# Kernel tuning notes

Hardware: AMD Instinct MI355X
Metric: run time of the kernel (lower is better)

Reference implementation:

```python
import jax, jax.numpy as jnp
import numpy as np

B, N, R, S, FIN, NCLS, KNN = 16, 2048, 64, 64, 6, 40, 40


def _knn_laplacian(x, k):
    # pairwise squared distance -> gaussian affinity -> row-wise top-k sparsify
    # -> symmetric-normalized Laplacian  L = I - D^{-1/2} A D^{-1/2}
    xx = jnp.sum(x * x, axis=-1)                      # [B,N]
    inner = jnp.einsum('bnd,bmd->bnm', x, x)          # [B,N,N]
    dist = xx[:, :, None] + xx[:, None, :] - 2.0 * inner
    A = jnp.exp(-dist)
    kth = jax.lax.top_k(A, k)[0][..., -1]             # k-th largest per row [B,N]
    A = jnp.where(A >= kth[..., None], A, jnp.zeros((), A.dtype))
    d = jnp.sum(A, axis=-1)
    dis = jnp.where(d > 0, jax.lax.rsqrt(jnp.maximum(d, 1e-12)), jnp.zeros((), A.dtype))
    L = jnp.eye(A.shape[-1], dtype=A.dtype) - dis[:, :, None] * A * dis[:, None, :]
    return L


def _cheb_conv(x, L, w, b):
    # DenseChebConv, K=3: T0=x, T1=Lx, T2=2LT1-T0, then linear on concat
    t0 = x
    t1 = jnp.matmul(L, x)
    t2 = 2.0 * jnp.matmul(L, t1) - t0
    xc = jnp.concatenate([t0, t1, t2], axis=-1)       # [B,N,3*Fin]
    return jnp.matmul(xc, w) + b


def setup_inputs() -> dict:
    key = jax.random.key(0)
    ks = jax.random.split(key, 16)
    p = lambda k_, sh: (jax.random.normal(k_, sh, dtype=jnp.float32) * 0.02)
    return {
        'x': jax.random.normal(ks[0], (B, N, FIN), dtype=jnp.float32),
        'laplacian_Reeb': jax.random.normal(ks[1], (B, R, R), dtype=jnp.float32),
        'sccs': jax.random.randint(ks[2], (B, R, S), 0, N),
        'vertices_reeb': jax.random.normal(ks[3], (B * R, 3), dtype=jnp.float32),
        'edges_reeb': jax.random.randint(ks[4], (B, 128, 2), 0, R),
        'labels': jax.random.randint(ks[5], (B,), 0, NCLS),
        'k': KNN, 'batch_size': B, 'num_points': N,
        'conv1_w': p(ks[6], (3 * FIN, 128)), 'conv1_b': jnp.zeros((128,), jnp.float32),
        'conv2_w': p(ks[7], (3 * 128, 512)), 'conv2_b': jnp.zeros((512,), jnp.float32),
        'convReeb_w': p(ks[8], (3 * 128, 512)), 'convReeb_b': jnp.zeros((512,), jnp.float32),
        'fc1_w': p(ks[9], (1024, 512)), 'fc1_b': jnp.zeros((512,), jnp.float32),
        'fc2_w': p(ks[10], (512, 128)), 'fc2_b': jnp.zeros((128,), jnp.float32),
        'fc3_w': p(ks[11], (128, NCLS)), 'fc3_b': jnp.zeros((NCLS,), jnp.float32),
    }


def reference(x, laplacian_Reeb, sccs, vertices_reeb, edges_reeb, labels, k,
              batch_size, num_points, conv1_w, conv1_b, conv2_w, conv2_b,
              convReeb_w, convReeb_b, fc1_w, fc1_b, fc2_w, fc2_b, fc3_w, fc3_b):
    regs = []
    # graph build is under no_grad in the original
    L = jax.lax.stop_gradient(_knn_laplacian(x, k))
    out = jax.nn.relu(_cheb_conv(x, L, conv1_w, conv1_b))           # [B,N,128]
    regs.append(jnp.linalg.norm(jnp.einsum('bnf,bnm,bmg->bfg', out, L, out)) ** 2)

    # Reeb ragged segment-max pool (no_grad in original): gather SCC index
    # groups per Reeb node and max-reduce -> [B,R,128]
    gathered = jax.vmap(lambda o, s: o[s])(out, sccs)               # [B,R,S,128]
    Vertices_final_Reeb = jax.lax.stop_gradient(jnp.max(gathered, axis=2))
    laplacian_Reeb_final = jax.lax.stop_gradient(laplacian_Reeb)

    L2 = jax.lax.stop_gradient(_knn_laplacian(out, k))
    out = jax.nn.relu(_cheb_conv(out, L2, conv2_w, conv2_b))        # [B,N,512]
    regs.append(jnp.linalg.norm(jnp.einsum('bnf,bnm,bmg->bfg', out, L2, out)) ** 2)

    out_Reeb = jax.nn.relu(_cheb_conv(Vertices_final_Reeb, laplacian_Reeb_final,
                                      convReeb_w, convReeb_b))      # [B,R,512]
    regs.append(jnp.linalg.norm(jnp.einsum('brf,brq,bqg->bfg', out_Reeb,
                                           laplacian_Reeb_final, out_Reeb)) ** 2)

    out = jnp.max(out, axis=1)            # [B,512]
    out_Reeb = jnp.max(out_Reeb, axis=1)  # [B,512]
    out = jnp.concatenate([out_Reeb, out], axis=1)                  # [B,1024]

    out = jnp.matmul(out, fc1_w) + fc1_b
    regs.append(jnp.linalg.norm(fc1_w[:, 0]) ** 2); regs.append(fc1_b[0] ** 2)
    out = jax.nn.relu(out)
    out = jnp.matmul(out, fc2_w) + fc2_b
    regs.append(jnp.linalg.norm(fc2_w[:, 0]) ** 2); regs.append(fc2_b[0] ** 2)
    out = jax.nn.relu(out)
    out = jnp.matmul(out, fc3_w) + fc3_b
    regs.append(jnp.linalg.norm(fc3_w[:, 0]) ** 2); regs.append(fc3_b[0] ** 2)
    return out, jnp.stack(regs)
```

## Files before the change

### kernel.cpp

```cpp
#include <hip/hip_runtime.h>

#define NB 16
#define NP 2048
#define NR 64
#define NS 64
#define KSEL 40

typedef __attribute__((ext_vector_type(8))) short bf16x8;
typedef __attribute__((ext_vector_type(4))) float f32x4;

constexpr long aOUT1 = 0;
constexpr long aT1A  = aOUT1 + 16L*2048*128;
constexpr long aT2A  = aT1A  + 16L*2048*6;
constexpr long aZ1   = aT2A  + 16L*2048*6;
constexpr long aVALS1= aZ1   + 16L*2048*128;
constexpr long aDIS1 = aVALS1+ 16L*2048*64;
constexpr long aVALS2= aDIS1 + 16L*2048;
constexpr long aDIS2 = aVALS2+ 16L*2048*64;
constexpr long aXX2  = aDIS2 + 16L*2048;
constexpr long aXX1  = aXX2  + 16L*2048;
constexpr long aT1B  = aXX1  + 16L*2048;
constexpr long aT2B  = aT1B  + 16L*2048*128;
constexpr long aOUT2 = aT2B  + 16L*2048*128;
constexpr long aZ2   = aOUT2 + 16L*2048*512;
constexpr long aVFR  = aZ2   + 16L*2048*512;
constexpr long aT1R  = aVFR  + 16L*64*128;
constexpr long aT2R  = aT1R  + 16L*64*128;
constexpr long aOUTR = aT2R  + 16L*64*128;
constexpr long aZR   = aOUTR + 16L*64*512;
constexpr long aPOOL = aZR   + 16L*64*512;
constexpr long aFC1O = aPOOL + 16L*1024;
constexpr long aFC2O = aFC1O + 16L*512;
constexpr long aMPP  = aFC2O + 16L*128;
constexpr long aM1P  = aMPP  + 16L*8*512;
constexpr long aM2P  = aM1P  + 8L*16*128*128;
constexpr long FTOT  = aM2P  + 4L*16*512*512;

constexpr long iCOLS1 = 0;
constexpr long iCNT1  = iCOLS1 + 16L*2048*64;
constexpr long iCOLS2 = iCNT1  + 16L*2048;
constexpr long iCNT2  = iCOLS2 + 16L*2048*64;
constexpr long ITOT   = iCNT2  + 16L*2048;

constexpr long uOUT1H = 0;
constexpr long uOUT1L = uOUT1H + 16L*2048*128;
constexpr long uOUT1R = uOUT1L + 16L*2048*128;
constexpr long uT1BH  = uOUT1R + 16L*2048*128;
constexpr long uT1BL  = uT1BH  + 16L*2048*128;
constexpr long uT2BH  = uT1BL  + 16L*2048*128;
constexpr long uT2BL  = uT2BH  + 16L*2048*128;
constexpr long uW2T   = uT2BL  + 16L*2048*128;
constexpr long uVFRH  = uW2T   + 512L*384;
constexpr long uVFRL  = uVFRH  + 16L*64*128;
constexpr long uT1RH  = uVFRL  + 16L*64*128;
constexpr long uT1RL  = uT1RH  + 16L*64*128;
constexpr long uT2RH  = uT1RL  + 16L*64*128;
constexpr long uT2RL  = uT2RH  + 16L*64*128;
constexpr long uWRT   = uT2RL  + 16L*64*128;
constexpr long uOUT1T = uWRT   + 512L*384;
constexpr long uZ1T   = uOUT1T + 16L*128*2048;
constexpr long uOUT2T = uZ1T   + 16L*128*2048;
constexpr long uZ2T   = uOUT2T + 16L*512*2048;
constexpr long uOUTRT = uZ2T   + 16L*512*2048;
constexpr long uZRT   = uOUTRT + 16L*512*64;
constexpr long uOUT2B = uZRT   + 16L*512*64;
constexpr long uG     = uOUT2B + 16L*2048*512;
constexpr long UTOT   = uG     + 16L*2048*2048;

__device__ __align__(256) float  g_farena[FTOT];
__device__ __align__(256) int    g_iarena[ITOT];
__device__ __align__(256) ushort g_uarena[UTOT];

__device__ __forceinline__ float wsum_f(float v){
  #pragma unroll
  for (int s=32;s>0;s>>=1) v += __shfl_xor(v, s, 64);
  return v;
}
__device__ __forceinline__ int wsum_i(int v){
  #pragma unroll
  for (int s=32;s>0;s>>=1) v += __shfl_xor(v, s, 64);
  return v;
}

__device__ __forceinline__ void gl2lds16(const void* g, void* l){
  __builtin_amdgcn_global_load_lds(
      (const __attribute__((address_space(1))) void*)g,
      (__attribute__((address_space(3))) void*)l, 16, 0, 0);
}

__device__ __forceinline__ ushort bf_rne(float x){
  unsigned u = __float_as_uint(x);
  u += 0x7fffu + ((u >> 16) & 1u);
  return (ushort)(u >> 16);
}
__device__ __forceinline__ void bf_hilo(float x, ushort& h, ushort& l){
  unsigned u = __float_as_uint(x);
  h = (ushort)(u >> 16);
  float hf = __uint_as_float(u & 0xffff0000u);
  l = (ushort)(__float_as_uint(x - hf) >> 16);
}
__device__ __forceinline__ float bf2f(ushort u){
  return __uint_as_float(((unsigned)u) << 16);
}

__device__ __forceinline__ void topk_store(float (&dk)[32], int lane, long row,
    int* __restrict__ cols, float* __restrict__ vals,
    int* __restrict__ cnt, float* __restrict__ dis)
{
  float dmin = dk[0], dmax = dk[0];
  #pragma unroll
  for (int q=1;q<32;++q){ dmin = fminf(dmin, dk[q]); dmax = fmaxf(dmax, dk[q]); }
  #pragma unroll
  for (int s=32;s>0;s>>=1){
    dmin = fminf(dmin, __shfl_xor(dmin, s, 64));
    dmax = fmaxf(dmax, __shfl_xor(dmax, s, 64));
  }
  int c0 = 0;
  #pragma unroll
  for (int q=0;q<32;++q) c0 += (int)__popcll(__ballot(dk[q] <= dmin));
  float kth;
  if (c0 >= KSEL){
    kth = dmin;
  } else {
    float lo = dmin, hi = dmax;
    int cLo = c0, cHi = 2048, it = 0;
    while (cHi != KSEL && __float_as_uint(hi) - __float_as_uint(lo) > 1u){
      float t;
      if (it & 1){
        t = __uint_as_float((__float_as_uint(lo) + __float_as_uint(hi)) >> 1);
      } else {
        t = lo + (hi - lo) * ((float)(KSEL - cLo) / (float)(cHi - cLo));
        unsigned tb = __float_as_uint(t);
        unsigned lb = __float_as_uint(lo), hb = __float_as_uint(hi);
        if (tb <= lb) tb = lb + 1u;
        else if (tb >= hb) tb = hb - 1u;
        t = __uint_as_float(tb);
      }
      ++it;
      int c = 0;
      #pragma unroll
      for (int q=0;q<32;++q) c += (int)__popcll(__ballot(dk[q] <= t));
      if (c >= KSEL){ hi = t; cHi = c; } else { lo = t; cLo = c; }
    }
    kth = hi;
  }
  int kc = 0;
  #pragma unroll
  for (int q=0;q<32;++q) kc += (dk[q] <= kth) ? 1 : 0;
  int tot = wsum_i(kc);
  int incl = kc;
  #pragma unroll
  for (int s=1;s<64;s<<=1){ int u = __shfl_up(incl, s, 64); if (lane >= s) incl += u; }
  int pos = incl - kc;
  int* cp = cols + row*64; float* vp = vals + row*64;
  float d = 0.f;
  #pragma unroll
  for (int q=0;q<32;++q){
    if (dk[q] <= kth){
      float v = __expf(-dk[q]);
      d += v;
      if (pos < 64){ cp[pos] = q*64 + lane; vp[pos] = v; }
      pos++;
    }
  }
  d = wsum_f(d);
  if (lane == 0){
    cnt[row] = tot <= 64 ? tot : 64;
    dis[row] = d > 0.f ? (1.0f / sqrtf(fmaxf(d, 1e-12f))) : 0.f;
  }
}

__global__ __launch_bounds__(256) void xx6_kernel(const float* __restrict__ x,
    float* __restrict__ xx1)
{
  long i = (long)blockIdx.x*256 + threadIdx.x;
  const float* p = x + i*6;
  float2 v0 = *(const float2*)(p);
  float2 v1 = *(const float2*)(p+2);
  float2 v2 = *(const float2*)(p+4);
  xx1[i] = v0.x*v0.x + v0.y*v0.y + v1.x*v1.x + v1.y*v1.y + v2.x*v2.x + v2.y*v2.y;
}

__global__ __launch_bounds__(256) void knn1_kernel(const float* __restrict__ x,
    const float* __restrict__ xx1,
    int* __restrict__ cols, float* __restrict__ vals, int* __restrict__ cnt,
    float* __restrict__ dis)
{
  int lane = threadIdx.x & 63;
  long row = (long)blockIdx.x*4 + (threadIdx.x >> 6);
  int b = (int)(row >> 11); int i = (int)(row & (NP-1));
  const float* xb = x + (long)b*NP*6;
  const float* xxb = xx1 + ((long)b << 11);
  float xi[6];
  #pragma unroll
  for (int d2=0; d2<6; ++d2) xi[d2] = xb[(long)i*6 + d2];
  float xxi = xxb[i];
  float dk[32];
  #pragma unroll 4
  for (int c=0;c<32;++c){
    int j = c*64 + lane;
    const float* xj = xb + (long)j*6;
    float2 v0 = *(const float2*)(xj);
    float2 v1 = *(const float2*)(xj+2);
    float2 v2 = *(const float2*)(xj+4);
    float inr = xi[0]*v0.x + xi[1]*v0.y + xi[2]*v1.x + xi[3]*v1.y + xi[4]*v2.x + xi[5]*v2.y;
    dk[c] = fmaxf(xxi + xxb[j] - 2.f*inr, 0.f);
  }
  topk_store(dk, lane, row, cols, vals, cnt, dis);
}

__global__ __launch_bounds__(256) void knn2_kernel(const ushort* __restrict__ G,
    const float* __restrict__ xx,
    int* __restrict__ cols, float* __restrict__ vals, int* __restrict__ cnt,
    float* __restrict__ dis)
{
  int lane = threadIdx.x & 63;
  long row = (long)blockIdx.x*4 + (threadIdx.x >> 6);
  const ushort* Gr = G + row*NP;
  const float* xxb = xx + ((row >> 11) << 11);
  int i = (int)(row & (NP-1));
  float xxi = xxb[i];
  float dk[32];
  #pragma unroll 4
  for (int c=0;c<32;++c){
    int j = c*64 + lane;
    dk[c] = fmaxf(xxi + xxb[j] - 2.f*bf2f(Gr[j]), 0.f);
  }
  topk_store(dk, lane, row, cols, vals, cnt, dis);
}

__global__ __launch_bounds__(256) void spmm6_kernel(const float* __restrict__ X,
    const float* __restrict__ T0, float* __restrict__ Y,
    const int* __restrict__ cols, const float* __restrict__ vals,
    const int* __restrict__ cnt, const float* __restrict__ dis,
    float c1, float c2, float cs)
{
  long row = (long)blockIdx.x*256 + threadIdx.x;
  int b = (int)(row >> 11);
  const float* Xb = X + ((long)b << 11)*6;
  const float* db = dis + ((long)b << 11);
  float acc[6] = {0,0,0,0,0,0};
  int c = cnt[row];
  const int* cp = cols + row*64; const float* vp = vals + row*64;
  for (int t=0;t<c;++t){
    int j = cp[t];
    float w = vp[t] * db[j];
    const float* xr = Xb + (long)j*6;
    #pragma unroll
    for (int d2=0; d2<6; ++d2) acc[d2] += w * xr[d2];
  }
  float di = dis[row];
  #pragma unroll
  for (int d2=0; d2<6; ++d2)
    Y[row*6+d2] = c1*X[row*6+d2] + c2*T0[row*6+d2] - cs*di*acc[d2];
}

template<int W, bool PACK>
__global__ __launch_bounds__((W >= 256) ? 256 : W) void spmm_kernel(
    const float* __restrict__ X, const float* __restrict__ T0, float* __restrict__ Y,
    ushort* __restrict__ Hh, ushort* __restrict__ Ll,
    const int* __restrict__ cols, const float* __restrict__ vals,
    const int* __restrict__ cnt, const float* __restrict__ dis,
    float c1, float c2, float cs)
{
  constexpr int TPB = (W >= 256) ? 256 : W;
  constexpr int E = W / TPB;
  __shared__ int scol[64];
  __shared__ float sval[64];
  int q = blockIdx.x;
  long row = ((long)(q & 7) << 12) + (q >> 3);
  int b = (int)(row >> 11);
  int tid = threadIdx.x;
  int c = cnt[row];
  if (tid < 64){ scol[tid] = cols[row*64+tid]; sval[tid] = vals[row*64+tid]; }
  __syncthreads();
  const float* Xb = X + ((long)b << 11)*W;
  const float* db = dis + ((long)b << 11);
  float acc[E] = {};
  for (int t=0;t<c;++t){
    int j = scol[t];
    float w = sval[t] * db[j];
    const float* xr = Xb + (long)j*W;
    #pragma unroll
    for (int e=0;e<E;++e) acc[e] += w * xr[tid + e*TPB];
  }
  float di = dis[row];
  #pragma unroll
  for (int e=0;e<E;++e){
    long idx = row*W + tid + e*TPB;
    float y = c1*X[idx] + c2*T0[idx] - cs*di*acc[e];
    Y[idx] = y;
    if (PACK){
      ushort h, l; bf_hilo(y, h, l);
      Hh[idx] = h; Ll[idx] = l;
    }
  }
}

__global__ __launch_bounds__(256) void spmmb_kernel(
    const float* __restrict__ X, const ushort* __restrict__ Xb,
    float* __restrict__ Y,
    const int* __restrict__ cols, const float* __restrict__ vals,
    const int* __restrict__ cnt, const float* __restrict__ dis)
{
  __shared__ int scol[4][64];
  __shared__ float sval[4][64];
  int q = blockIdx.x;
  int wid = threadIdx.x >> 6, lane = threadIdx.x & 63;
  long row = ((long)(q & 7) << 12) + ((long)(q >> 3) << 2) + wid;
  int b = (int)(row >> 11);
  scol[wid][lane] = cols[row*64 + lane];
  sval[wid][lane] = vals[row*64 + lane];
  const ushort* Xbb = Xb + ((long)b << 11)*512;
  const float* db = dis + ((long)b << 11);
  int c = cnt[row];
  float acc[8] = {};
  for (int t=0;t<c;++t){
    int j = scol[wid][t];
    float w = sval[wid][t] * db[j];
    bf16x8 v = *(const bf16x8*)(Xbb + (long)j*512 + lane*8);
    #pragma unroll
    for (int e=0;e<8;++e)
      acc[e] += w * bf2f((ushort)v[e]);
  }
  float di = dis[row];
  long base = row*512 + lane*8;
  float4 x0 = *(const float4*)(X + base);
  float4 x1 = *(const float4*)(X + base + 4);
  float4 o0, o1;
  o0.x = x0.x - di*acc[0]; o0.y = x0.y - di*acc[1];
  o0.z = x0.z - di*acc[2]; o0.w = x0.w - di*acc[3];
  o1.x = x1.x - di*acc[4]; o1.y = x1.y - di*acc[5];
  o1.z = x1.z - di*acc[6]; o1.w = x1.w - di*acc[7];
  *(float4*)(Y + base) = o0;
  *(float4*)(Y + base + 4) = o1;
}

__global__ __launch_bounds__(128) void conv1_kernel(const float* __restrict__ x,
    const float* __restrict__ t1, const float* __restrict__ t2,
    const float* __restrict__ w, const float* __restrict__ bias,
    float* __restrict__ out, ushort* __restrict__ oh, ushort* __restrict__ ol,
    ushort* __restrict__ orr)
{
  long row = blockIdx.x; int o = threadIdx.x;
  float acc = bias[o];
  const float* xr = x + row*6; const float* a1 = t1 + row*6; const float* a2 = t2 + row*6;
  #pragma unroll
  for (int d2=0; d2<6; ++d2){
    acc += xr[d2]*w[d2*128 + o];
    acc += a1[d2]*w[(6+d2)*128 + o];
    acc += a2[d2]*w[(12+d2)*128 + o];
  }
  acc = fmaxf(acc, 0.f);
  long idx = row*128 + o;
  out[idx] = acc;
  ushort h, l; bf_hilo(acc, h, l);
  oh[idx] = h; ol[idx] = l;
  orr[idx] = bf_rne(acc);
}

template<bool HILO>
__global__ __launch_bounds__(256) void tpack_kernel(const float* __restrict__ X,
    ushort* __restrict__ H, ushort* __restrict__ L,
    int R, int C, long sIn, long sOut)
{
  __shared__ float tile[32][33];
  int c0 = blockIdx.x*32, r0 = blockIdx.y*32, b = blockIdx.z;
  const float* Xb = X + (long)b*sIn;
  int tx = threadIdx.x & 31, ty = threadIdx.x >> 5;
  #pragma unroll
  for (int rr=ty; rr<32; rr+=8)
    tile[rr][tx] = Xb[(long)(r0+rr)*C + c0+tx];
  __syncthreads();
  #pragma unroll
  for (int cc=ty; cc<32; cc+=8){
    float xv = tile[tx][cc];
    long oidx = (long)b*sOut + (long)(c0+cc)*R + r0 + tx;
    if (HILO){
      ushort h, l; bf_hilo(xv, h, l);
      H[oidx] = h; L[oidx] = l;
    } else {
      H[oidx] = bf_rne(xv);
    }
  }
}

template<bool SPLITA, bool CHEB, bool BR>
__global__ __launch_bounds__(256) void mgemm_kernel(
    const ushort* __restrict__ Ah0, const ushort* __restrict__ Ah1, const ushort* __restrict__ Ah2,
    const ushort* __restrict__ Al0, const ushort* __restrict__ Al1, const ushort* __restrict__ Al2,
    const ushort* __restrict__ Bh,
    const float* __restrict__ bias, float* __restrict__ C,
    ushort* __restrict__ Cb, float* __restrict__ ssq,
    int M, int N, int K, long sA, long sB, long sC,
    int kchunk, long sSplit)
{
  __shared__ ushort AsH[128*32];
  __shared__ ushort BsH[128*32];
  __shared__ ushort AsL[SPLITA ? 128*32 : 8];
  int bz = blockIdx.z;
  int kb = 0, ke = K;
  long coff = 0;
  if (kchunk > 0){
    int split = bz >> 4; bz &= 15;
    kb = split * kchunk;
    ke = kb + kchunk; if (ke > K) ke = K;
    coff = (long)split * sSplit;
  }
  int m0 = blockIdx.x*128, n0 = blockIdx.y*128;
  int tid = threadIdx.x, lane = tid & 63, wid = tid >> 6;
  int wm = (wid & 1)*64, wn = (wid >> 1)*64;
  f32x4 acc[4][4] = {};
  const ushort* Bb = Bh + (long)bz*sB;
  const ushort* Ab = CHEB ? Ah0 : (Ah0 + (long)bz*sA);
  const ushort* Alb = (SPLITA && !CHEB) ? (Al0 + (long)bz*sA) : Al0;

  for (int k0 = kb; k0 < ke; k0 += 32){
    #pragma unroll
    for (int cc2=0; cc2<2; ++cc2){
      int chunk = wid*2 + cc2;
      int e = chunk*512 + lane*8;
      int row = e >> 5;
      int slot = (e >> 3) & 3;
      int scol = (slot ^ ((row >> 1) & 3)) * 8;
      const ushort* asrc;
      if (CHEB){
        int kg2 = k0 + scol;
        const ushort* base = (kg2 < 128) ? Ah0 : ((kg2 < 256) ? Ah1 : Ah2);
        asrc = base + (long)(m0+row)*128 + (kg2 & 127);
      } else {
        asrc = Ab + (long)(m0+row)*K + k0 + scol;
      }
      gl2lds16(asrc, &AsH[chunk*512]);
      gl2lds16(Bb + (long)(n0+row)*K + k0 + scol, &BsH[chunk*512]);
      if (SPLITA){
        const ushort* alsrc;
        if (CHEB){
          int kg2 = k0 + scol;
          const ushort* base = (kg2 < 128) ? Al0 : ((kg2 < 256) ? Al1 : Al2);
          alsrc = base + (long)(m0+row)*128 + (kg2 & 127);
        } else {
          alsrc = Alb + (long)(m0+row)*K + k0 + scol;
        }
        gl2lds16(alsrc, &AsL[chunk*512]);
      }
    }
    __syncthreads();
    int lr = lane & 15, kg = lane >> 4;
    bf16x8 af[4], bfr[4];
    #pragma unroll
    for (int f=0; f<4; ++f){
      int ra = wm + f*16 + lr;
      int rb = wn + f*16 + lr;
      af[f]  = *(const bf16x8*)&AsH[ra*32 + (kg ^ ((ra>>1)&3))*8];
      bfr[f] = *(const bf16x8*)&BsH[rb*32 + (kg ^ ((rb>>1)&3))*8];
    }
    if (SPLITA){
      bf16x8 al[4];
      #pragma unroll
      for (int f=0; f<4; ++f){
        int ra = wm + f*16 + lr;
        al[f] = *(const bf16x8*)&AsL[ra*32 + (kg ^ ((ra>>1)&3))*8];
      }
      #pragma unroll
      for (int mf=0; mf<4; ++mf)
        #pragma unroll
        for (int nf=0; nf<4; ++nf){
          acc[mf][nf] = __builtin_amdgcn_mfma_f32_16x16x32_bf16(af[mf], bfr[nf], acc[mf][nf], 0,0,0);
          acc[mf][nf] = __builtin_amdgcn_mfma_f32_16x16x32_bf16(al[mf], bfr[nf], acc[mf][nf], 0,0,0);
        }
    } else {
      #pragma unroll
      for (int mf=0; mf<4; ++mf)
        #pragma unroll
        for (int nf=0; nf<4; ++nf)
          acc[mf][nf] = __builtin_amdgcn_mfma_f32_16x16x32_bf16(af[mf], bfr[nf], acc[mf][nf], 0,0,0);
    }
    __syncthreads();
  }
  int lr = lane & 15, l4 = (lane >> 4)*4;
  if (ssq){
    float s = 0.f;
    #pragma unroll
    for (int mf=0; mf<4; ++mf)
      #pragma unroll
      for (int nf=0; nf<4; ++nf)
        #pragma unroll
        for (int r=0; r<4; ++r){ float v = acc[mf][nf][r]; s += v*v; }
    s = wsum_f(s);
    if (lane == 0) atomicAdd(ssq, s);
    return;
  }
  #pragma unroll
  for (int mf=0; mf<4; ++mf){
    #pragma unroll
    for (int nf=0; nf<4; ++nf){
      int n = n0 + wn + nf*16 + lr;
      float bv = BR ? bias[n] : 0.f;
      #pragma unroll
      for (int r=0; r<4; ++r){
        int m = m0 + wm + mf*16 + l4 + r;
        float v = acc[mf][nf][r];
        if (BR) v = fmaxf(v + bv, 0.f);
        if (C)  C[coff + (long)bz*sC + (long)m*N + n] = v;
        if (Cb) Cb[(long)bz*sC + (long)m*N + n] = bf_rne(v);
      }
    }
  }
}

__global__ __launch_bounds__(256) void redssq_kernel(const float* __restrict__ P,
    long n, int S, long stride, float* __restrict__ tgt)
{
  __shared__ float ps[4];
  float s = 0.f;
  for (long i = (long)blockIdx.x*256 + threadIdx.x; i < n; i += (long)gridDim.x*256){
    float v = 0.f;
    for (int q=0;q<S;++q) v += P[i + (long)q*stride];
    s += v*v;
  }
  s = wsum_f(s);
  int lane = threadIdx.x & 63, wid = threadIdx.x >> 6;
  if (lane == 0) ps[wid] = s;
  __syncthreads();
  if (threadIdx.x == 0) atomicAdd(tgt, ps[0]+ps[1]+ps[2]+ps[3]);
}

__global__ __launch_bounds__(256) void rownorm_kernel(const float* __restrict__ X,
    float* __restrict__ xx)
{
  int lane = threadIdx.x & 63;
  long row = (long)blockIdx.x*4 + (threadIdx.x >> 6);
  const float* p = X + row*128;
  float v0 = p[lane], v1 = p[64+lane];
  float s = wsum_f(v0*v0 + v1*v1);
  if (lane == 0) xx[row] = s;
}

__global__ __launch_bounds__(128) void reeb_pool_kernel(const float* __restrict__ out1,
    const int* __restrict__ sccs, float* __restrict__ VfR,
    ushort* __restrict__ Hh, ushort* __restrict__ Ll)
{
  int q = blockIdx.x;
  int br = ((q & 7) << 7) + (q >> 3);
  int b = br >> 6;
  int f = threadIdx.x;
  const int* sp = sccs + (long)br*NS;
  const float* ob = out1 + ((long)b << 11)*128;
  float m = -1e30f;
  for (int s=0;s<NS;++s){
    int idx = sp[s];
    m = fmaxf(m, ob[(long)idx*128 + f]);
  }
  long oidx = (long)br*128 + f;
  VfR[oidx] = m;
  ushort h, l; bf_hilo(m, h, l);
  Hh[oidx] = h; Ll[oidx] = l;
}

template<int W, bool PACK>
__global__ __launch_bounds__((W>=256)?256:W) void reeb_mm_kernel(const float* __restrict__ Lap,
    const float* __restrict__ X, const float* __restrict__ T0, float* __restrict__ Y,
    ushort* __restrict__ Hh, ushort* __restrict__ Ll,
    float cs, float c2)
{
  constexpr int TPB = (W>=256)?256:W;
  constexpr int E = W/TPB;
  int br = blockIdx.x; int b = br >> 6; int r = br & 63;
  const float* lr = Lap + ((long)b*NR + r)*NR;
  const float* Xb = X + (long)b*NR*W;
  int tid = threadIdx.x;
  float acc[E] = {};
  for (int q=0;q<NR;++q){
    float w = lr[q];
    #pragma unroll
    for (int e=0;e<E;++e) acc[e] += w * Xb[(long)q*W + tid + e*TPB];
  }
  #pragma unroll
  for (int e=0;e<E;++e){
    long idx = (long)br*W + tid + e*TPB;
    float y = cs*acc[e] + c2*T0[idx];
    Y[idx] = y;
    if (PACK){
      ushort h, l; bf_hilo(y, h, l);
      Hh[idx] = h; Ll[idx] = l;
    }
  }
}

__global__ __launch_bounds__(512) void maxpool1_kernel(const float* __restrict__ X,
    float* __restrict__ part)
{
  int b = blockIdx.x, rc = blockIdx.y; int f = threadIdx.x;
  const float* p = X + ((long)b*2048 + (long)rc*256)*512 + f;
  float m = -1e30f;
  #pragma unroll 4
  for (int r=0;r<256;++r) m = fmaxf(m, p[(long)r*512]);
  part[((long)b*8+rc)*512 + f] = m;
}

__global__ __launch_bounds__(512) void maxpool2_kernel(const float* __restrict__ part,
    const float* __restrict__ outR, float* __restrict__ pool)
{
  int b = blockIdx.x; int f = threadIdx.x;
  const float* pp = part + (long)b*8*512 + f;
  float m = -1e30f;
  #pragma unroll
  for (int r=0;r<8;++r) m = fmaxf(m, pp[r*512]);
  pool[(long)b*1024 + 512 + f] = m;
  const float* rp = outR + (long)b*64*512 + f;
  float mr = -1e30f;
  #pragma unroll 4
  for (int r=0;r<64;++r) mr = fmaxf(mr, rp[(long)r*512]);
  pool[(long)b*1024 + f] = mr;
}

template<bool RELU>
__global__ __launch_bounds__(256) void fc_kernel(const float* __restrict__ in,
    const float* __restrict__ W, const float* __restrict__ bias,
    float* __restrict__ out, int IN, int OUT)
{
  __shared__ float red[4][64];
  int b = blockIdx.x, o0 = blockIdx.y*64;
  int tid = threadIdx.x;
  int ol = tid & 63, q = tid >> 6;
  int o = o0 + ol;
  const float* ip = in + (long)b*IN;
  float acc = 0.f;
  if (o < OUT){
    int kb = IN >> 2;
    int ks = q*kb;
    for (int i=0;i<kb;i+=8){
      #pragma unroll
      for (int u=0;u<8;++u){
        int k = ks + i + u;
        acc += ip[k]*W[(long)k*OUT + o];
      }
    }
  }
  red[q][ol] = acc;
  __syncthreads();
  if (tid < 64){
    int oo = o0 + tid;
    if (oo < OUT){
      float s = red[0][tid]+red[1][tid]+red[2][tid]+red[3][tid] + bias[oo];
      out[(long)b*OUT + oo] = RELU ? fmaxf(s, 0.f) : s;
    }
  }
}

__global__ __launch_bounds__(256) void wreg_kernel(const float* __restrict__ w1,
    const float* __restrict__ b1, const float* __restrict__ w2, const float* __restrict__ b2,
    const float* __restrict__ w3, const float* __restrict__ b3, float* __restrict__ out9)
{
  __shared__ float ps[3][4];
  int tid = threadIdx.x, lane = tid & 63, wid = tid >> 6;
  float s1 = 0.f, s2 = 0.f, s3 = 0.f;
  for (int i=tid;i<1024;i+=256){ float v = w1[(long)i*512]; s1 += v*v; }
  for (int i=tid;i<512;i+=256){ float v = w2[(long)i*128]; s2 += v*v; }
  if (tid < 128){ float v = w3[(long)tid*40]; s3 = v*v; }
  s1 = wsum_f(s1); s2 = wsum_f(s2); s3 = wsum_f(s3);
  if (lane == 0){ ps[0][wid]=s1; ps[1][wid]=s2; ps[2][wid]=s3; }
  __syncthreads();
  if (tid == 0){
    out9[3] = ps[0][0]+ps[0][1]+ps[0][2]+ps[0][3];
    out9[4] = b1[0]*b1[0];
    out9[5] = ps[1][0]+ps[1][1]+ps[1][2]+ps[1][3];
    out9[6] = b2[0]*b2[0];
    out9[7] = ps[2][0]+ps[2][1]+ps[2][2]+ps[2][3];
    out9[8] = b3[0]*b3[0];
  }
}

extern "C" void kernel_launch(void* const* d_in, const int* in_sizes, int n_in,
                              void* d_out, int out_size, void* d_ws, size_t ws_size,
                              hipStream_t stream)
{
  (void)in_sizes; (void)n_in; (void)d_ws; (void)ws_size; (void)out_size;
  const float* x    = (const float*)d_in[0];
  const float* lapR = (const float*)d_in[1];
  const int*   sccs = (const int*)d_in[2];
  const float* w1   = (const float*)d_in[9];
  const float* b1   = (const float*)d_in[10];
  const float* w2   = (const float*)d_in[11];
  const float* b2   = (const float*)d_in[12];
  const float* wR   = (const float*)d_in[13];
  const float* bRb  = (const float*)d_in[14];
  const float* fw1  = (const float*)d_in[15];
  const float* fb1  = (const float*)d_in[16];
  const float* fw2  = (const float*)d_in[17];
  const float* fb2  = (const float*)d_in[18];
  const float* fw3  = (const float*)d_in[19];
  const float* fb3  = (const float*)d_in[20];
  float* out = (float*)d_out;

  float* Fb = nullptr; int* Ib = nullptr; ushort* Ub = nullptr;
  hipGetSymbolAddress((void**)&Fb, HIP_SYMBOL(g_farena));
  hipGetSymbolAddress((void**)&Ib, HIP_SYMBOL(g_iarena));
  hipGetSymbolAddress((void**)&Ub, HIP_SYMBOL(g_uarena));

  float* out1 = Fb + aOUT1;  float* t1a = Fb + aT1A;  float* t2a = Fb + aT2A;
  float* Z1   = Fb + aZ1;
  float* vals1= Fb + aVALS1; float* dis1= Fb + aDIS1;
  float* vals2= Fb + aVALS2; float* dis2= Fb + aDIS2;
  float* xx2  = Fb + aXX2;   float* xx1 = Fb + aXX1;
  float* t1b  = Fb + aT1B;   float* t2b = Fb + aT2B;
  float* out2 = Fb + aOUT2;  float* Z2  = Fb + aZ2;
  float* VfR  = Fb + aVFR;   float* t1R = Fb + aT1R;  float* t2R= Fb + aT2R;
  float* outR = Fb + aOUTR;  float* ZR  = Fb + aZR;
  float* pool = Fb + aPOOL;  float* fc1o= Fb + aFC1O; float* fc2o=Fb + aFC2O;
  float* mpp  = Fb + aMPP;   float* M1p = Fb + aM1P;  float* M2p = Fb + aM2P;
  int* cols1 = Ib + iCOLS1; int* cnt1 = Ib + iCNT1;
  int* cols2 = Ib + iCOLS2; int* cnt2 = Ib + iCNT2;
  ushort* out1h = Ub + uOUT1H; ushort* out1l = Ub + uOUT1L;
  ushort* out1r = Ub + uOUT1R;
  ushort* t1bh  = Ub + uT1BH;  ushort* t1bl  = Ub + uT1BL;
  ushort* t2bh  = Ub + uT2BH;  ushort* t2bl  = Ub + uT2BL;
  ushort* w2t   = Ub + uW2T;
  ushort* vfrh  = Ub + uVFRH;  ushort* vfrl  = Ub + uVFRL;
  ushort* t1rh  = Ub + uT1RH;  ushort* t1rl  = Ub + uT1RL;
  ushort* t2rh  = Ub + uT2RH;  ushort* t2rl  = Ub + uT2RL;
  ushort* wrt   = Ub + uWRT;
  ushort* out1t = Ub + uOUT1T; ushort* z1t   = Ub + uZ1T;
  ushort* out2t = Ub + uOUT2T; ushort* z2t   = Ub + uZ2T;
  ushort* outrt = Ub + uOUTRT; ushort* zrt   = Ub + uZRT;
  ushort* out2b = Ub + uOUT2B; ushort* Gb16  = Ub + uG;

  hipMemsetAsync(out + 640, 0, 9*sizeof(float), stream);

  xx6_kernel<<<dim3(128),dim3(256),0,stream>>>(x, xx1);
  knn1_kernel<<<dim3(8192),dim3(256),0,stream>>>(x, xx1, cols1, vals1, cnt1, dis1);
  spmm6_kernel<<<dim3(128),dim3(256),0,stream>>>(x, x, t1a, cols1, vals1, cnt1, dis1, 1.f, 0.f, 1.f);
  spmm6_kernel<<<dim3(128),dim3(256),0,stream>>>(t1a, x, t2a, cols1, vals1, cnt1, dis1, 2.f, -1.f, 2.f);
  conv1_kernel<<<dim3(32768),dim3(128),0,stream>>>(x, t1a, t2a, w1, b1, out1, out1h, out1l, out1r);

  spmm_kernel<128,false><<<dim3(32768),dim3(128),0,stream>>>(out1, out1, Z1, nullptr, nullptr,
      cols1, vals1, cnt1, dis1, 1.f, 0.f, 1.f);
  tpack_kernel<false><<<dim3(4,64,16),dim3(256),0,stream>>>(out1, out1t, nullptr, 2048,128, 2048L*128, 128L*2048);
  tpack_kernel<false><<<dim3(4,64,16),dim3(256),0,stream>>>(Z1,   z1t,   nullptr, 2048,128, 2048L*128, 128L*2048);
  mgemm_kernel<false,false,false><<<dim3(1,1,128),dim3(256),0,stream>>>(
      out1t,nullptr,nullptr, nullptr,nullptr,nullptr, z1t, nullptr, M1p,
      nullptr, nullptr, 128,128,2048, 128L*2048, 128L*2048, 128L*128, 256, 16L*128*128);
  redssq_kernel<<<dim3(512),dim3(256),0,stream>>>(M1p, 16L*128*128, 8, 16L*128*128, out+640);
  reeb_pool_kernel<<<dim3(1024),dim3(128),0,stream>>>(out1, sccs, VfR, vfrh, vfrl);

  rownorm_kernel<<<dim3(8192),dim3(256),0,stream>>>(out1, xx2);
  mgemm_kernel<false,false,false><<<dim3(16,16,16),dim3(256),0,stream>>>(
      out1r,nullptr,nullptr, nullptr,nullptr,nullptr, out1r, nullptr, nullptr,
      Gb16, nullptr, 2048,2048,128, (long)NP*128, (long)NP*128, (long)NP*NP, 0, 0);
  knn2_kernel<<<dim3(8192),dim3(256),0,stream>>>(Gb16, xx2, cols2, vals2, cnt2, dis2);

  spmm_kernel<128,true><<<dim3(32768),dim3(128),0,stream>>>(out1, out1, t1b, t1bh, t1bl,
      cols2, vals2, cnt2, dis2, 1.f, 0.f, 1.f);
  spmm_kernel<128,true><<<dim3(32768),dim3(128),0,stream>>>(t1b, out1, t2b, t2bh, t2bl,
      cols2, vals2, cnt2, dis2, 2.f, -1.f, 2.f);
  tpack_kernel<false><<<dim3(16,12,1),dim3(256),0,stream>>>(w2, w2t, nullptr, 384,512, 0,0);
  mgemm_kernel<true,true,true><<<dim3(256,4,1),dim3(256),0,stream>>>(
      out1h,t1bh,t2bh, out1l,t1bl,t2bl, w2t, b2, out2,
      out2b, nullptr, 32768,512,384, 0,0,0, 0, 0);
  spmmb_kernel<<<dim3(8192),dim3(256),0,stream>>>(out2, out2b, Z2, cols2, vals2, cnt2, dis2);
  tpack_kernel<false><<<dim3(16,64,16),dim3(256),0,stream>>>(out2, out2t, nullptr, 2048,512, 2048L*512, 512L*2048);
  tpack_kernel<false><<<dim3(16,64,16),dim3(256),0,stream>>>(Z2,   z2t,   nullptr, 2048,512, 2048L*512, 512L*2048);
  mgemm_kernel<false,false,false><<<dim3(4,4,64),dim3(256),0,stream>>>(
      out2t,nullptr,nullptr, nullptr,nullptr,nullptr, z2t, nullptr, M2p,
      nullptr, nullptr, 512,512,2048, 512L*2048, 512L*2048, 512L*512, 512, 16L*512*512);
  redssq_kernel<<<dim3(512),dim3(256),0,stream>>>(M2p, 16L*512*512, 4, 16L*512*512, out+641);

  reeb_mm_kernel<128,true><<<dim3(1024),dim3(128),0,stream>>>(lapR, VfR, VfR, t1R, t1rh, t1rl, 1.f, 0.f);
  reeb_mm_kernel<128,true><<<dim3(1024),dim3(128),0,stream>>>(lapR, t1R, VfR, t2R, t2rh, t2rl, 2.f, -1.f);
  tpack_kernel<false><<<dim3(16,12,1),dim3(256),0,stream>>>(wR, wrt, nullptr, 384,512, 0,0);
  mgemm_kernel<true,true,true><<<dim3(8,4,1),dim3(256),0,stream>>>(
      vfrh,t1rh,t2rh, vfrl,t1rl,t2rl, wrt, bRb, outR,
      nullptr, nullptr, 1024,512,384, 0,0,0, 0, 0);
  reeb_mm_kernel<512,false><<<dim3(1024),dim3(256),0,stream>>>(lapR, outR, outR, ZR, nullptr, nullptr, 1.f, 0.f);
  tpack_kernel<false><<<dim3(16,2,16),dim3(256),0,stream>>>(outR, outrt, nullptr, 64,512, 64L*512, 512L*64);
  tpack_kernel<false><<<dim3(16,2,16),dim3(256),0,stream>>>(ZR,   zrt,   nullptr, 64,512, 64L*512, 512L*64);
  mgemm_kernel<false,false,false><<<dim3(4,4,16),dim3(256),0,stream>>>(
      outrt,nullptr,nullptr, nullptr,nullptr,nullptr, zrt, nullptr, nullptr,
      nullptr, out+642, 512,512,64, 512L*64, 512L*64, 0, 0, 0);

  maxpool1_kernel<<<dim3(16,8),dim3(512),0,stream>>>(out2, mpp);
  maxpool2_kernel<<<dim3(16),dim3(512),0,stream>>>(mpp, outR, pool);
  fc_kernel<true ><<<dim3(16,8),dim3(256),0,stream>>>(pool, fw1, fb1, fc1o, 1024, 512);
  fc_kernel<true ><<<dim3(16,2),dim3(256),0,stream>>>(fc1o, fw2, fb2, fc2o, 512, 128);
  fc_kernel<false><<<dim3(16,1),dim3(256),0,stream>>>(fc2o, fw3, fb3, out, 128, 40);
  wreg_kernel<<<dim3(1),dim3(256),0,stream>>>(fw1, fb1, fw2, fb2, fw3, fb3, out+640);
}
```

Baseline: 1.058 ms.

## Keep conv2 output and Laplacian products in bf16, fuse FC layers

Stops writing the fp32 conv2 output and fp32 Z1/Z2 intermediates. The bf16 copies now feed the sparse matmul, the transposes (a new 16-bit transpose kernel) and the max-pool directly. The three FC launches are fused into one kernel, and the memset is folded into the first kernel. This cuts large fp32 write and read traffic and a few launches, at the cost of extra bf16 rounding on the Z2 path and on the pooled activations.

```diff
diff --git a/kernel.cpp b/kernel.cpp
--- a/kernel.cpp
+++ b/kernel.cpp
@@ -12,26 +12,21 @@
 constexpr long aOUT1 = 0;
 constexpr long aT1A  = aOUT1 + 16L*2048*128;
 constexpr long aT2A  = aT1A  + 16L*2048*6;
-constexpr long aZ1   = aT2A  + 16L*2048*6;
-constexpr long aVALS1= aZ1   + 16L*2048*128;
+constexpr long aXX2  = aT2A  + 16L*2048*6;
+constexpr long aXX1  = aXX2  + 16L*2048;
+constexpr long aVALS1= aXX1  + 16L*2048;
 constexpr long aDIS1 = aVALS1+ 16L*2048*64;
 constexpr long aVALS2= aDIS1 + 16L*2048;
 constexpr long aDIS2 = aVALS2+ 16L*2048*64;
-constexpr long aXX2  = aDIS2 + 16L*2048;
-constexpr long aXX1  = aXX2  + 16L*2048;
-constexpr long aT1B  = aXX1  + 16L*2048;
+constexpr long aT1B  = aDIS2 + 16L*2048;
 constexpr long aT2B  = aT1B  + 16L*2048*128;
-constexpr long aOUT2 = aT2B  + 16L*2048*128;
-constexpr long aZ2   = aOUT2 + 16L*2048*512;
-constexpr long aVFR  = aZ2   + 16L*2048*512;
+constexpr long aVFR  = aT2B  + 16L*2048*128;
 constexpr long aT1R  = aVFR  + 16L*64*128;
 constexpr long aT2R  = aT1R  + 16L*64*128;
 constexpr long aOUTR = aT2R  + 16L*64*128;
 constexpr long aZR   = aOUTR + 16L*64*512;
 constexpr long aPOOL = aZR   + 16L*64*512;
-constexpr long aFC1O = aPOOL + 16L*1024;
-constexpr long aFC2O = aFC1O + 16L*512;
-constexpr long aMPP  = aFC2O + 16L*128;
+constexpr long aMPP  = aPOOL + 16L*1024;
 constexpr long aM1P  = aMPP  + 16L*8*512;
 constexpr long aM2P  = aM1P  + 8L*16*128*128;
 constexpr long FTOT  = aM2P  + 4L*16*512*512;
@@ -65,7 +60,9 @@
 constexpr long uZRT   = uOUTRT + 16L*512*64;
 constexpr long uOUT2B = uZRT   + 16L*512*64;
 constexpr long uG     = uOUT2B + 16L*2048*512;
-constexpr long UTOT   = uG     + 16L*2048*2048;
+constexpr long uZ1B   = uG     + 16L*2048*2048;
+constexpr long uZ2B   = uZ1B   + 16L*2048*128;
+constexpr long UTOT   = uZ2B   + 16L*2048*512;
 
 __device__ __align__(256) float  g_farena[FTOT];
 __device__ __align__(256) int    g_iarena[ITOT];
@@ -171,8 +168,9 @@
 }
 
 __global__ __launch_bounds__(256) void xx6_kernel(const float* __restrict__ x,
-    float* __restrict__ xx1)
-{
+    float* __restrict__ xx1, float* __restrict__ reg3)
+{
+  if (blockIdx.x == 0 && threadIdx.x < 3) reg3[threadIdx.x] = 0.f;
   long i = (long)blockIdx.x*256 + threadIdx.x;
   const float* p = x + i*6;
   float2 v0 = *(const float2*)(p);
@@ -255,7 +253,7 @@
     Y[row*6+d2] = c1*X[row*6+d2] + c2*T0[row*6+d2] - cs*di*acc[d2];
 }
 
-template<int W, bool PACK>
+template<int W, int PMODE, bool WY>
 __global__ __launch_bounds__((W >= 256) ? 256 : W) void spmm_kernel(
     const float* __restrict__ X, const float* __restrict__ T0, float* __restrict__ Y,
     ushort* __restrict__ Hh, ushort* __restrict__ Ll,
@@ -289,17 +287,18 @@
   for (int e=0;e<E;++e){
     long idx = row*W + tid + e*TPB;
     float y = c1*X[idx] + c2*T0[idx] - cs*di*acc[e];
-    Y[idx] = y;
-    if (PACK){
+    if (WY) Y[idx] = y;
+    if (PMODE == 1){
       ushort h, l; bf_hilo(y, h, l);
       Hh[idx] = h; Ll[idx] = l;
+    } else if (PMODE == 2){
+      Hh[idx] = bf_rne(y);
     }
   }
 }
 
 __global__ __launch_bounds__(256) void spmmb_kernel(
-    const float* __restrict__ X, const ushort* __restrict__ Xb,
-    float* __restrict__ Y,
+    const ushort* __restrict__ Xb, ushort* __restrict__ Yb,
     const int* __restrict__ cols, const float* __restrict__ vals,
     const int* __restrict__ cnt, const float* __restrict__ dis)
 {
@@ -325,15 +324,12 @@
   }
   float di = dis[row];
   long base = row*512 + lane*8;
-  float4 x0 = *(const float4*)(X + base);
-  float4 x1 = *(const float4*)(X + base + 4);
-  float4 o0, o1;
-  o0.x = x0.x - di*acc[0]; o0.y = x0.y - di*acc[1];
-  o0.z = x0.z - di*acc[2]; o0.w = x0.w - di*acc[3];
-  o1.x = x1.x - di*acc[4]; o1.y = x1.y - di*acc[5];
-  o1.z = x1.z - di*acc[6]; o1.w = x1.w - di*acc[7];
-  *(float4*)(Y + base) = o0;
-  *(float4*)(Y + base + 4) = o1;
+  bf16x8 xv = *(const bf16x8*)(Xb + base);
+  bf16x8 o;
+  #pragma unroll
+  for (int e=0;e<8;++e)
+    o[e] = (short)bf_rne(bf2f((ushort)xv[e]) - di*acc[e]);
+  *(bf16x8*)(Yb + base) = o;
 }
 
 __global__ __launch_bounds__(128) void conv1_kernel(const float* __restrict__ x,
@@ -383,6 +379,22 @@
       H[oidx] = bf_rne(xv);
     }
   }
+}
+
+__global__ __launch_bounds__(256) void tpack16_kernel(const ushort* __restrict__ In,
+    ushort* __restrict__ Out, int R, int C, long sIn, long sOut)
+{
+  __shared__ ushort tile[32][33];
+  int c0 = blockIdx.x*32, r0 = blockIdx.y*32, b = blockIdx.z;
+  const ushort* Ib = In + (long)b*sIn;
+  int tx = threadIdx.x & 31, ty = threadIdx.x >> 5;
+  #pragma unroll
+  for (int rr=ty; rr<32; rr+=8)
+    tile[rr][tx] = Ib[(long)(r0+rr)*C + c0+tx];
+  __syncthreads();
+  #pragma unroll
+  for (int cc=ty; cc<32; cc+=8)
+    Out[(long)b*sOut + (long)(c0+cc)*R + r0 + tx] = tile[tx][cc];
 }
 
 template<bool SPLITA, bool CHEB, bool BR>
@@ -588,14 +600,14 @@
   }
 }
 
-__global__ __launch_bounds__(512) void maxpool1_kernel(const float* __restrict__ X,
+__global__ __launch_bounds__(512) void maxpool1_kernel(const ushort* __restrict__ Xb,
     float* __restrict__ part)
 {
   int b = blockIdx.x, rc = blockIdx.y; int f = threadIdx.x;
-  const float* p = X + ((long)b*2048 + (long)rc*256)*512 + f;
+  const ushort* p = Xb + ((long)b*2048 + (long)rc*256)*512 + f;
   float m = -1e30f;
   #pragma unroll 4
-  for (int r=0;r<256;++r) m = fmaxf(m, p[(long)r*512]);
+  for (int r=0;r<256;++r) m = fmaxf(m, bf2f(p[(long)r*512]));
   part[((long)b*8+rc)*512 + f] = m;
 }
 
@@ -615,37 +627,42 @@
   pool[(long)b*1024 + f] = mr;
 }
 
-template<bool RELU>
-__global__ __launch_bounds__(256) void fc_kernel(const float* __restrict__ in,
-    const float* __restrict__ W, const float* __restrict__ bias,
-    float* __restrict__ out, int IN, int OUT)
-{
-  __shared__ float red[4][64];
-  int b = blockIdx.x, o0 = blockIdx.y*64;
-  int tid = threadIdx.x;
-  int ol = tid & 63, q = tid >> 6;
-  int o = o0 + ol;
-  const float* ip = in + (long)b*IN;
-  float acc = 0.f;
-  if (o < OUT){
-    int kb = IN >> 2;
-    int ks = q*kb;
-    for (int i=0;i<kb;i+=8){
+__global__ __launch_bounds__(256) void fcall_kernel(const float* __restrict__ pool,
+    const float* __restrict__ fw1, const float* __restrict__ fb1,
+    const float* __restrict__ fw2, const float* __restrict__ fb2,
+    const float* __restrict__ fw3, const float* __restrict__ fb3,
+    float* __restrict__ out)
+{
+  __shared__ float in_s[1024];
+  __shared__ float h1[512];
+  __shared__ float h2[128];
+  int b = blockIdx.x, tid = threadIdx.x;
+  for (int i=tid;i<1024;i+=256) in_s[i] = pool[(long)b*1024 + i];
+  __syncthreads();
+  float a0 = fb1[tid], a1 = fb1[tid+256];
+  for (int k=0;k<1024;k+=4){
+    #pragma unroll
+    for (int u=0;u<4;++u){
+      float v = in_s[k+u];
+      a0 += v*fw1[(long)(k+u)*512 + tid];
+      a1 += v*fw1[(long)(k+u)*512 + tid+256];
+    }
+  }
+  h1[tid] = fmaxf(a0, 0.f); h1[tid+256] = fmaxf(a1, 0.f);
+  __syncthreads();
+  if (tid < 128){
+    float a = fb2[tid];
+    for (int k=0;k<512;k+=4){
       #pragma unroll
-      for (int u=0;u<8;++u){
-        int k = ks + i + u;
-        acc += ip[k]*W[(long)k*OUT + o];
-      }
-    }
-  }
-  red[q][ol] = acc;
+      for (int u=0;u<4;++u) a += h1[k+u]*fw2[(long)(k+u)*128 + tid];
+    }
+    h2[tid] = fmaxf(a, 0.f);
+  }
   __syncthreads();
-  if (tid < 64){
-    int oo = o0 + tid;
-    if (oo < OUT){
-      float s = red[0][tid]+red[1][tid]+red[2][tid]+red[3][tid] + bias[oo];
-      out[(long)b*OUT + oo] = RELU ? fmaxf(s, 0.f) : s;
-    }
+  if (tid < 40){
+    float a = fb3[tid];
+    for (int k=0;k<128;++k) a += h2[k]*fw3[(long)k*40 + tid];
+    out[(long)b*40 + tid] = a;
   }
 }
 
@@ -700,15 +717,13 @@
   hipGetSymbolAddress((void**)&Ub, HIP_SYMBOL(g_uarena));
 
   float* out1 = Fb + aOUT1;  float* t1a = Fb + aT1A;  float* t2a = Fb + aT2A;
-  float* Z1   = Fb + aZ1;
   float* vals1= Fb + aVALS1; float* dis1= Fb + aDIS1;
   float* vals2= Fb + aVALS2; float* dis2= Fb + aDIS2;
   float* xx2  = Fb + aXX2;   float* xx1 = Fb + aXX1;
   float* t1b  = Fb + aT1B;   float* t2b = Fb + aT2B;
-  float* out2 = Fb + aOUT2;  float* Z2  = Fb + aZ2;
   float* VfR  = Fb + aVFR;   float* t1R = Fb + aT1R;  float* t2R= Fb + aT2R;
   float* outR = Fb + aOUTR;  float* ZR  = Fb + aZR;
-  float* pool = Fb + aPOOL;  float* fc1o= Fb + aFC1O; float* fc2o=Fb + aFC2O;
+  float* pool = Fb + aPOOL;
   float* mpp  = Fb + aMPP;   float* M1p = Fb + aM1P;  float* M2p = Fb + aM2P;
   int* cols1 = Ib + iCOLS1; int* cnt1 = Ib + iCNT1;
   int* cols2 = Ib + iCOLS2; int* cnt2 = Ib + iCNT2;
@@ -725,19 +740,18 @@
   ushort* out2t = Ub + uOUT2T; ushort* z2t   = Ub + uZ2T;
   ushort* outrt = Ub + uOUTRT; ushort* zrt   = Ub + uZRT;
   ushort* out2b = Ub + uOUT2B; ushort* Gb16  = Ub + uG;
-
-  hipMemsetAsync(out + 640, 0, 9*sizeof(float), stream);
-
-  xx6_kernel<<<dim3(128),dim3(256),0,stream>>>(x, xx1);
+  ushort* z1b   = Ub + uZ1B;   ushort* z2b   = Ub + uZ2B;
+
+  xx6_kernel<<<dim3(128),dim3(256),0,stream>>>(x, xx1, out+640);
   knn1_kernel<<<dim3(8192),dim3(256),0,stream>>>(x, xx1, cols1, vals1, cnt1, dis1);
   spmm6_kernel<<<dim3(128),dim3(256),0,stream>>>(x, x, t1a, cols1, vals1, cnt1, dis1, 1.f, 0.f, 1.f);
   spmm6_kernel<<<dim3(128),dim3(256),0,stream>>>(t1a, x, t2a, cols1, vals1, cnt1, dis1, 2.f, -1.f, 2.f);
   conv1_kernel<<<dim3(32768),dim3(128),0,stream>>>(x, t1a, t2a, w1, b1, out1, out1h, out1l, out1r);
 
-  spmm_kernel<128,false><<<dim3(32768),dim3(128),0,stream>>>(out1, out1, Z1, nullptr, nullptr,
+  spmm_kernel<128,2,false><<<dim3(32768),dim3(128),0,stream>>>(out1, out1, nullptr, z1b, nullptr,
       cols1, vals1, cnt1, dis1, 1.f, 0.f, 1.f);
-  tpack_kernel<false><<<dim3(4,64,16),dim3(256),0,stream>>>(out1, out1t, nullptr, 2048,128, 2048L*128, 128L*2048);
-  tpack_kernel<false><<<dim3(4,64,16),dim3(256),0,stream>>>(Z1,   z1t,   nullptr, 2048,128, 2048L*128, 128L*2048);
+  tpack16_kernel<<<dim3(4,64,16),dim3(256),0,stream>>>(out1r, out1t, 2048,128, 2048L*128, 128L*2048);
+  tpack16_kernel<<<dim3(4,64,16),dim3(256),0,stream>>>(z1b,   z1t,   2048,128, 2048L*128, 128L*2048);
   mgemm_kernel<false,false,false><<<dim3(1,1,128),dim3(256),0,stream>>>(
       out1t,nullptr,nullptr, nullptr,nullptr,nullptr, z1t, nullptr, M1p,
       nullptr, nullptr, 128,128,2048, 128L*2048, 128L*2048, 128L*128, 256, 16L*128*128);
@@ -750,17 +764,17 @@
       Gb16, nullptr, 2048,2048,128, (long)NP*128, (long)NP*128, (long)NP*NP, 0, 0);
   knn2_kernel<<<dim3(8192),dim3(256),0,stream>>>(Gb16, xx2, cols2, vals2, cnt2, dis2);
 
-  spmm_kernel<128,true><<<dim3(32768),dim3(128),0,stream>>>(out1, out1, t1b, t1bh, t1bl,
+  spmm_kernel<128,1,true><<<dim3(32768),dim3(128),0,stream>>>(out1, out1, t1b, t1bh, t1bl,
       cols2, vals2, cnt2, dis2, 1.f, 0.f, 1.f);
-  spmm_kernel<128,true><<<dim3(32768),dim3(128),0,stream>>>(t1b, out1, t2b, t2bh, t2bl,
+  spmm_kernel<128,1,true><<<dim3(32768),dim3(128),0,stream>>>(t1b, out1, t2b, t2bh, t2bl,
       cols2, vals2, cnt2, dis2, 2.f, -1.f, 2.f);
   tpack_kernel<false><<<dim3(16,12,1),dim3(256),0,stream>>>(w2, w2t, nullptr, 384,512, 0,0);
   mgemm_kernel<true,true,true><<<dim3(256,4,1),dim3(256),0,stream>>>(
-      out1h,t1bh,t2bh, out1l,t1bl,t2bl, w2t, b2, out2,
-      out2b, nullptr, 32768,512,384, 0,0,0, 0, 0);
-  spmmb_kernel<<<dim3(8192),dim3(256),0,stream>>>(out2, out2b, Z2, cols2, vals2, cnt2, dis2);
-  tpack_kernel<false><<<dim3(16,64,16),dim3(256),0,stream>>>(out2, out2t, nullptr, 2048,512, 2048L*512, 512L*2048);
-  tpack_kernel<false><<<dim3(16,64,16),dim3(256),0,stream>>>(Z2,   z2t,   nullptr, 2048,512, 2048L*512, 512L*2048);
+      out1h,t1bh,t2bh, out1l,t1bl,t2bl, w2t, b2, nullptr,
+      out2b, nullptr, 32768,512,384, 0,0, 2048L*512, 0, 0);
+  spmmb_kernel<<<dim3(8192),dim3(256),0,stream>>>(out2b, z2b, cols2, vals2, cnt2, dis2);
+  tpack16_kernel<<<dim3(16,64,16),dim3(256),0,stream>>>(out2b, out2t, 2048,512, 2048L*512, 512L*2048);
+  tpack16_kernel<<<dim3(16,64,16),dim3(256),0,stream>>>(z2b,   z2t,   2048,512, 2048L*512, 512L*2048);
   mgemm_kernel<false,false,false><<<dim3(4,4,64),dim3(256),0,stream>>>(
       out2t,nullptr,nullptr, nullptr,nullptr,nullptr, z2t, nullptr, M2p,
       nullptr, nullptr, 512,512,2048, 512L*2048, 512L*2048, 512L*512, 512, 16L*512*512);
@@ -779,10 +793,8 @@
       outrt,nullptr,nullptr, nullptr,nullptr,nullptr, zrt, nullptr, nullptr,
       nullptr, out+642, 512,512,64, 512L*64, 512L*64, 0, 0, 0);
 
-  maxpool1_kernel<<<dim3(16,8),dim3(512),0,stream>>>(out2, mpp);
+  maxpool1_kernel<<<dim3(16,8),dim3(512),0,stream>>>(out2b, mpp);
   maxpool2_kernel<<<dim3(16),dim3(512),0,stream>>>(mpp, outR, pool);
-  fc_kernel<true ><<<dim3(16,8),dim3(256),0,stream>>>(pool, fw1, fb1, fc1o, 1024, 512);
-  fc_kernel<true ><<<dim3(16,2),dim3(256),0,stream>>>(fc1o, fw2, fb2, fc2o, 512, 128);
-  fc_kernel<false><<<dim3(16,1),dim3(256),0,stream>>>(fc2o, fw3, fb3, out, 128, 40);
+  fcall_kernel<<<dim3(16),dim3(256),0,stream>>>(pool, fw1, fb1, fw2, fb2, fw3, fb3, out);
   wreg_kernel<<<dim3(1),dim3(256),0,stream>>>(fw1, fb1, fw2, fb2, fw3, fb3, out+640);
 }
```

After: 1.096 ms. 3.6% more time.
